# Performance work log

Measured on AMD Instinct MI355X. Metric: run time of the kernel, lower is better.

Reference implementation:

```python
import jax, jax.numpy as jnp
import numpy as np

N = 100000      # nodes
E = 1600000     # edges (avg degree 16)
IN = 128        # in_channels == nf
NF = 128        # hidden width
OUT = 3         # out_channels
NEG = 0.02      # LeakyReLU slope
EPS = 1e-5      # GraphNorm eps


def setup_inputs() -> dict:
    key = jax.random.key(0)
    ks = jax.random.split(key, 12)
    x = jax.random.normal(ks[0], (N, IN), dtype=jnp.float32)
    edge_index = jax.random.randint(ks[1], (2, E), 0, N, dtype=jnp.int32)
    s = 1.0 / np.sqrt(NF)
    # 6 hidden SAGEConv layers (NF->NF), stacked
    Wl = jax.random.normal(ks[2], (6, NF, NF), dtype=jnp.float32) * s
    bl = jnp.zeros((6, NF), dtype=jnp.float32)
    Wr = jax.random.normal(ks[3], (6, NF, NF), dtype=jnp.float32) * s
    # final SAGEConv NF -> OUT
    Wl_out = jax.random.normal(ks[4], (OUT, NF), dtype=jnp.float32) * s
    bl_out = jnp.zeros((OUT,), dtype=jnp.float32)
    Wr_out = jax.random.normal(ks[5], (OUT, NF), dtype=jnp.float32) * s
    # GraphNorm params for the 6 hidden layers
    gamma = jnp.ones((6, NF), dtype=jnp.float32)
    beta = jnp.zeros((6, NF), dtype=jnp.float32)
    alpha = jnp.ones((6, NF), dtype=jnp.float32)  # mean_scale
    return {"x": x, "edge_index": edge_index, "Wl": Wl, "bl": bl, "Wr": Wr,
            "Wl_out": Wl_out, "bl_out": bl_out, "Wr_out": Wr_out,
            "gamma": gamma, "beta": beta, "alpha": alpha}


def _sage_conv(h, src, dst, W_l, b_l, W_r):
    # max-aggregate messages x_j = h[src] onto dst, then two linears
    m = jax.ops.segment_max(h[src], dst, num_segments=h.shape[0])
    m = jnp.where(jnp.isfinite(m), m, 0.0)  # empty segments -> 0
    return m @ W_l.T + b_l + h @ W_r.T


def _graph_norm(h, g, b, a):
    mean = jnp.mean(h, axis=0, keepdims=True)          # [1, NF]
    sub = h - a * mean
    var = jnp.mean(sub * sub, axis=0, keepdims=True)   # [1, NF]
    return g * sub * jax.lax.rsqrt(var + EPS) + b


def reference(x, edge_index, Wl, bl, Wr, Wl_out, bl_out, Wr_out, gamma, beta, alpha):
    src, dst = edge_index[0], edge_index[1]
    h = x
    for i in range(6):
        h = _sage_conv(h, src, dst, Wl[i], bl[i], Wr[i])
        h = _graph_norm(h, gamma[i], beta[i], alpha[i])
        h = jnp.where(h > 0, h, NEG * h)  # LeakyReLU(0.02); dropout p=0
    h = _sage_conv(h, src, dst, Wl_out, bl_out, Wr_out)
    return jnp.tanh(h) * 0.5
```

## Files before the change

kernel.cpp:

```cpp
#include <hip/hip_runtime.h>
#include <math.h>

#define NN 100000
#define NE 1600000
#define NF 128
#define NOUT 3
#define NEGS 0.02f
#define GEPS 1e-5f

typedef __attribute__((ext_vector_type(8))) short bf16x8;
typedef __attribute__((ext_vector_type(4))) float f32x4;

__device__ __forceinline__ unsigned short bf16_rn(float f) {
    unsigned u = __float_as_uint(f);
    unsigned r = u + 0x7FFFu + ((u >> 16) & 1u);
    return (unsigned short)(r >> 16);
}
__device__ __forceinline__ float bf16_tf(unsigned short h) {
    return __uint_as_float((unsigned)h << 16);
}
__device__ __forceinline__ unsigned pk2(float v) {
    unsigned short hi = bf16_rn(v);
    unsigned short lo = bf16_rn(v - bf16_tf(hi));
    return ((unsigned)hi << 16) | lo;
}
__device__ __forceinline__ float unpk(unsigned u) {
    return __uint_as_float(u & 0xFFFF0000u) + __uint_as_float(u << 16);
}

__global__ void k_hist(const int* __restrict__ dst, int* __restrict__ counts,
                       int* __restrict__ rank) {
    int i = blockIdx.x * blockDim.x + threadIdx.x;
    if (i < NE) rank[i] = atomicAdd(&counts[dst[i]], 1);
}

__global__ void k_scan1(const int* __restrict__ counts, int* __restrict__ bsums) {
    __shared__ int s[256];
    int i = blockIdx.x * 256 + threadIdx.x;
    s[threadIdx.x] = (i < NN) ? counts[i] : 0;
    __syncthreads();
    for (int off = 128; off > 0; off >>= 1) {
        if (threadIdx.x < off) s[threadIdx.x] += s[threadIdx.x + off];
        __syncthreads();
    }
    if (threadIdx.x == 0) bsums[blockIdx.x] = s[0];
}

__global__ void k_scan2(int* __restrict__ bsums, int nb) {
    __shared__ int s[512];
    int t = threadIdx.x;
    int v = (t < nb) ? bsums[t] : 0;
    s[t] = v;
    __syncthreads();
    for (int off = 1; off < 512; off <<= 1) {
        int u = (t >= off) ? s[t - off] : 0;
        __syncthreads();
        s[t] += u;
        __syncthreads();
    }
    if (t < nb) bsums[t] = s[t] - v;
}

__global__ void k_scan3(const int* __restrict__ counts, const int* __restrict__ bsums,
                        int* __restrict__ offsets) {
    __shared__ int s[256];
    int i = blockIdx.x * 256 + threadIdx.x;
    int v = (i < NN) ? counts[i] : 0;
    s[threadIdx.x] = v;
    __syncthreads();
    for (int off = 1; off < 256; off <<= 1) {
        int u = (threadIdx.x >= off) ? s[threadIdx.x - off] : 0;
        __syncthreads();
        s[threadIdx.x] += u;
        __syncthreads();
    }
    int excl = s[threadIdx.x] - v + bsums[blockIdx.x];
    if (i <= NN) offsets[i] = excl;
}

__global__ void k_scatter(const int* __restrict__ src, const int* __restrict__ dst,
                          const int* __restrict__ offsets, const int* __restrict__ rank,
                          int* __restrict__ csr) {
    int i = blockIdx.x * blockDim.x + threadIdx.x;
    if (i < NE) csr[offsets[dst[i]] + rank[i]] = src[i];
}

__global__ void k_wsplit(const float* __restrict__ Wl, const float* __restrict__ Wr,
                         unsigned short* __restrict__ whi, unsigned short* __restrict__ wlo) {
    int i = blockIdx.x * 256 + threadIdx.x;
    if (i >= 6 * NF * 256) return;
    int L = i >> 15;
    int rem = i & 32767;
    int o = rem >> 8;
    int k = rem & 255;
    float v = (k < NF) ? Wl[L * NF * NF + o * NF + k] : Wr[L * NF * NF + o * NF + (k - NF)];
    unsigned short h = bf16_rn(v);
    whi[i] = h;
    wlo[i] = bf16_rn(v - bf16_tf(h));
}

__global__ void k_xpack(const float* __restrict__ x, unsigned* __restrict__ hpk) {
    int i = blockIdx.x * 256 + threadIdx.x;
    float4 v = ((const float4*)x)[i];
    uint4 p;
    p.x = pk2(v.x); p.y = pk2(v.y); p.z = pk2(v.z); p.w = pk2(v.w);
    ((uint4*)hpk)[i] = p;
}

__global__ __launch_bounds__(256) void k_aggmax(const unsigned* __restrict__ hpk,
                                                const int* __restrict__ offsets,
                                                const int* __restrict__ csr,
                                                unsigned* __restrict__ mpk) {
    int node = blockIdx.x * 4 + (threadIdx.x >> 6);
    int l = threadIdx.x & 63;
    int beg = offsets[node], end = offsets[node + 1];
    float aa = -INFINITY, ab = -INFINITY;
    int e = beg;
    for (; e + 8 <= end; e += 8) {
        int s0 = csr[e],     s1 = csr[e + 1], s2 = csr[e + 2], s3 = csr[e + 3];
        int s4 = csr[e + 4], s5 = csr[e + 5], s6 = csr[e + 6], s7 = csr[e + 7];
        uint2 g0 = *(const uint2*)&hpk[(size_t)s0 * NF + 2 * l];
        uint2 g1 = *(const uint2*)&hpk[(size_t)s1 * NF + 2 * l];
        uint2 g2 = *(const uint2*)&hpk[(size_t)s2 * NF + 2 * l];
        uint2 g3 = *(const uint2*)&hpk[(size_t)s3 * NF + 2 * l];
        uint2 g4 = *(const uint2*)&hpk[(size_t)s4 * NF + 2 * l];
        uint2 g5 = *(const uint2*)&hpk[(size_t)s5 * NF + 2 * l];
        uint2 g6 = *(const uint2*)&hpk[(size_t)s6 * NF + 2 * l];
        uint2 g7 = *(const uint2*)&hpk[(size_t)s7 * NF + 2 * l];
        float m0 = fmaxf(fmaxf(unpk(g0.x), unpk(g1.x)), fmaxf(unpk(g2.x), unpk(g3.x)));
        float m1 = fmaxf(fmaxf(unpk(g4.x), unpk(g5.x)), fmaxf(unpk(g6.x), unpk(g7.x)));
        float n0 = fmaxf(fmaxf(unpk(g0.y), unpk(g1.y)), fmaxf(unpk(g2.y), unpk(g3.y)));
        float n1 = fmaxf(fmaxf(unpk(g4.y), unpk(g5.y)), fmaxf(unpk(g6.y), unpk(g7.y)));
        aa = fmaxf(aa, fmaxf(m0, m1));
        ab = fmaxf(ab, fmaxf(n0, n1));
    }
    for (; e + 4 <= end; e += 4) {
        int s0 = csr[e], s1 = csr[e + 1], s2 = csr[e + 2], s3 = csr[e + 3];
        uint2 g0 = *(const uint2*)&hpk[(size_t)s0 * NF + 2 * l];
        uint2 g1 = *(const uint2*)&hpk[(size_t)s1 * NF + 2 * l];
        uint2 g2 = *(const uint2*)&hpk[(size_t)s2 * NF + 2 * l];
        uint2 g3 = *(const uint2*)&hpk[(size_t)s3 * NF + 2 * l];
        aa = fmaxf(aa, fmaxf(fmaxf(unpk(g0.x), unpk(g1.x)), fmaxf(unpk(g2.x), unpk(g3.x))));
        ab = fmaxf(ab, fmaxf(fmaxf(unpk(g0.y), unpk(g1.y)), fmaxf(unpk(g2.y), unpk(g3.y))));
    }
    for (; e < end; ++e) {
        uint2 g = *(const uint2*)&hpk[(size_t)csr[e] * NF + 2 * l];
        aa = fmaxf(aa, unpk(g.x));
        ab = fmaxf(ab, unpk(g.y));
    }
    uint2 r;
    r.x = (beg == end) ? 0u : pk2(aa);
    r.y = (beg == end) ? 0u : pk2(ab);
    *(uint2*)&mpk[(size_t)node * NF + 2 * l] = r;
}

__global__ __launch_bounds__(512) void k_gemm(const unsigned* __restrict__ mpk,
                                              const unsigned* __restrict__ hpk,
                                              const unsigned short* __restrict__ whi,
                                              const unsigned short* __restrict__ wlo,
                                              const float* __restrict__ bias,
                                              unsigned* __restrict__ zpk,
                                              float* __restrict__ stats) {
    __shared__ __align__(16) unsigned short wlds[32768];
    __shared__ float redS[64], redQ[64];
    const int tid = threadIdx.x;
    const int half = blockIdx.y;
    const int w = tid >> 6;
    const int l = tid & 63;
    const int arow = l & 15;
    const int kg = l >> 4;

    if (tid < 64) { redS[tid] = 0.f; redQ[tid] = 0.f; }

#pragma unroll
    for (int i = 0; i < 8; i++) {
        int gd = tid + i * 512;
        int arr = gd >> 11;
        int rem = gd & 2047;
        int nt = rem >> 9;
        int ks = (rem >> 6) & 7;
        int ls = rem & 63;
        int r = nt * 16 + (ls & 15);
        int g = ks * 4 + (ls >> 4);
        const unsigned short* srcw = arr ? wlo : whi;
        bf16x8 v = *(const bf16x8*)&srcw[(size_t)(half * 64 + r) * 256 + g * 8];
        *(bf16x8*)&wlds[arr * 16384 + rem * 8] = v;
    }
    __syncthreads();

    const int nbase = blockIdx.x * 256 + w * 32;
    int an0 = nbase + arow;      if (an0 > NN - 1) an0 = NN - 1;
    int an1 = nbase + 16 + arow; if (an1 > NN - 1) an1 = NN - 1;

    f32x4 acc0[4], acc1[4];
#pragma unroll
    for (int nt = 0; nt < 4; nt++) {
        acc0[nt] = (f32x4){0.f, 0.f, 0.f, 0.f};
        acc1[nt] = (f32x4){0.f, 0.f, 0.f, 0.f};
    }

    union U { uint4 u; bf16x8 v; };

#pragma unroll
    for (int ks = 0; ks < 8; ks++) {
        const unsigned* A = (ks < 4) ? mpk : hpk;
        const int ak = (ks & 3) * 32 + kg * 8;
        uint4 p0 = *(const uint4*)&A[(size_t)an0 * NF + ak];
        uint4 p1 = *(const uint4*)&A[(size_t)an0 * NF + ak + 4];
        uint4 q0 = *(const uint4*)&A[(size_t)an1 * NF + ak];
        uint4 q1 = *(const uint4*)&A[(size_t)an1 * NF + ak + 4];

        U ah0, al0, ah1, al1;
        ah0.u.x = (p0.x >> 16) | (p0.y & 0xFFFF0000u);
        ah0.u.y = (p0.z >> 16) | (p0.w & 0xFFFF0000u);
        ah0.u.z = (p1.x >> 16) | (p1.y & 0xFFFF0000u);
        ah0.u.w = (p1.z >> 16) | (p1.w & 0xFFFF0000u);
        al0.u.x = (p0.x & 0xFFFFu) | (p0.y << 16);
        al0.u.y = (p0.z & 0xFFFFu) | (p0.w << 16);
        al0.u.z = (p1.x & 0xFFFFu) | (p1.y << 16);
        al0.u.w = (p1.z & 0xFFFFu) | (p1.w << 16);
        ah1.u.x = (q0.x >> 16) | (q0.y & 0xFFFF0000u);
        ah1.u.y = (q0.z >> 16) | (q0.w & 0xFFFF0000u);
        ah1.u.z = (q1.x >> 16) | (q1.y & 0xFFFF0000u);
        ah1.u.w = (q1.z >> 16) | (q1.w & 0xFFFF0000u);
        al1.u.x = (q0.x & 0xFFFFu) | (q0.y << 16);
        al1.u.y = (q0.z & 0xFFFFu) | (q0.w << 16);
        al1.u.z = (q1.x & 0xFFFFu) | (q1.y << 16);
        al1.u.w = (q1.z & 0xFFFFu) | (q1.w << 16);

        bf16x8 bh[4], bl[4];
#pragma unroll
        for (int nt = 0; nt < 4; nt++) {
            int el = (nt * 512 + ks * 64 + l) * 8;
            bh[nt] = *(const bf16x8*)&wlds[el];
            bl[nt] = *(const bf16x8*)&wlds[16384 + el];
        }
#pragma unroll
        for (int nt = 0; nt < 4; nt++) {
            acc0[nt] = __builtin_amdgcn_mfma_f32_16x16x32_bf16(ah0.v, bh[nt], acc0[nt], 0, 0, 0);
            acc1[nt] = __builtin_amdgcn_mfma_f32_16x16x32_bf16(ah1.v, bh[nt], acc1[nt], 0, 0, 0);
        }
#pragma unroll
        for (int nt = 0; nt < 4; nt++) {
            acc0[nt] = __builtin_amdgcn_mfma_f32_16x16x32_bf16(ah0.v, bl[nt], acc0[nt], 0, 0, 0);
            acc1[nt] = __builtin_amdgcn_mfma_f32_16x16x32_bf16(ah1.v, bl[nt], acc1[nt], 0, 0, 0);
        }
#pragma unroll
        for (int nt = 0; nt < 4; nt++) {
            acc0[nt] = __builtin_amdgcn_mfma_f32_16x16x32_bf16(al0.v, bh[nt], acc0[nt], 0, 0, 0);
            acc1[nt] = __builtin_amdgcn_mfma_f32_16x16x32_bf16(al1.v, bh[nt], acc1[nt], 0, 0, 0);
        }
    }

#pragma unroll
    for (int nt = 0; nt < 4; nt++) {
        const int f = half * 64 + nt * 16 + arow;
        const float b = bias[f];
        float s = 0.f, q = 0.f;
#pragma unroll
        for (int r = 0; r < 4; r++) {
            int n0 = nbase + kg * 4 + r;
            float v0 = acc0[nt][r] + b;
            if (n0 < NN) { zpk[(size_t)n0 * NF + f] = pk2(v0); s += v0; q += v0 * v0; }
            int n1 = nbase + 16 + kg * 4 + r;
            float v1 = acc1[nt][r] + b;
            if (n1 < NN) { zpk[(size_t)n1 * NF + f] = pk2(v1); s += v1; q += v1 * v1; }
        }
        s += __shfl_xor(s, 16); s += __shfl_xor(s, 32);
        q += __shfl_xor(q, 16); q += __shfl_xor(q, 32);
        if (l < 16) {
            atomicAdd(&redS[nt * 16 + l], s);
            atomicAdd(&redQ[nt * 16 + l], q);
        }
    }
    __syncthreads();
    if (tid < 64) {
        atomicAdd(&stats[half * 64 + tid], redS[tid]);
        atomicAdd(&stats[NF + half * 64 + tid], redQ[tid]);
    }
}

__global__ __launch_bounds__(256) void k_norm(const float* __restrict__ stats,
                                              const float* __restrict__ gamma,
                                              const float* __restrict__ beta,
                                              const float* __restrict__ alpha,
                                              const unsigned* __restrict__ zpk,
                                              unsigned* __restrict__ hpk) {
    __shared__ float sc[NF], sh[NF];
    int tid = threadIdx.x;
    if (tid < NF) {
        float mean = stats[tid] * (1.0f / NN);
        float ex2 = stats[NF + tid] * (1.0f / NN);
        float a = alpha[tid];
        float am = a * mean;
        float var = ex2 - 2.f * am * mean + am * am;
        float inv = rsqrtf(var + GEPS);
        float g = gamma[tid] * inv;
        sc[tid] = g;
        sh[tid] = beta[tid] - g * am;
    }
    __syncthreads();
    int i = blockIdx.x * 256 + tid;
    uint4 z = ((const uint4*)zpk)[i];
    int f = (i & 31) * 4;
    float r0 = sc[f + 0] * unpk(z.x) + sh[f + 0]; r0 = r0 > 0.f ? r0 : NEGS * r0;
    float r1 = sc[f + 1] * unpk(z.y) + sh[f + 1]; r1 = r1 > 0.f ? r1 : NEGS * r1;
    float r2 = sc[f + 2] * unpk(z.z) + sh[f + 2]; r2 = r2 > 0.f ? r2 : NEGS * r2;
    float r3 = sc[f + 3] * unpk(z.w) + sh[f + 3]; r3 = r3 > 0.f ? r3 : NEGS * r3;
    uint4 p;
    p.x = pk2(r0); p.y = pk2(r1); p.z = pk2(r2); p.w = pk2(r3);
    ((uint4*)hpk)[i] = p;
}

__global__ __launch_bounds__(256) void k_final(const unsigned* __restrict__ mpk,
                                               const unsigned* __restrict__ hpk,
                                               const float* __restrict__ Wlo_,
                                               const float* __restrict__ blo_,
                                               const float* __restrict__ Wro_,
                                               float* __restrict__ out) {
    __shared__ __align__(16) float W[NOUT][256];
    __shared__ float bb[NOUT];
    int tid = threadIdx.x;
    for (int i = tid; i < NOUT * 256; i += 256) {
        int o = i >> 8, k = i & 255;
        W[o][k] = (k < NF) ? Wlo_[o * NF + k] : Wro_[o * NF + (k - NF)];
    }
    if (tid < NOUT) bb[tid] = blo_[tid];
    __syncthreads();

    int node = blockIdx.x * 64 + (tid >> 2);
    int j = tid & 3;
    if (node >= NN) return;
    const unsigned* sp = (j < 2) ? mpk : hpk;
    int kbase = (j & 1) * 64;
    const unsigned* rp = &sp[(size_t)node * NF + kbase];
    float a0 = 0.f, a1 = 0.f, a2 = 0.f;
#pragma unroll
    for (int q = 0; q < 16; q++) {
        uint4 u = *(const uint4*)&rp[q * 4];
        float v0 = unpk(u.x), v1 = unpk(u.y), v2 = unpk(u.z), v3 = unpk(u.w);
        int k = j * 64 + q * 4;
        float4 w0 = *(const float4*)&W[0][k];
        float4 w1 = *(const float4*)&W[1][k];
        float4 w2 = *(const float4*)&W[2][k];
        a0 += v0 * w0.x + v1 * w0.y + v2 * w0.z + v3 * w0.w;
        a1 += v0 * w1.x + v1 * w1.y + v2 * w1.z + v3 * w1.w;
        a2 += v0 * w2.x + v1 * w2.y + v2 * w2.z + v3 * w2.w;
    }
    a0 += __shfl_down(a0, 2, 4); a0 += __shfl_down(a0, 1, 4);
    a1 += __shfl_down(a1, 2, 4); a1 += __shfl_down(a1, 1, 4);
    a2 += __shfl_down(a2, 2, 4); a2 += __shfl_down(a2, 1, 4);
    if (j == 0) {
        out[node * 3 + 0] = tanhf(a0 + bb[0]) * 0.5f;
        out[node * 3 + 1] = tanhf(a1 + bb[1]) * 0.5f;
        out[node * 3 + 2] = tanhf(a2 + bb[2]) * 0.5f;
    }
}

extern "C" void kernel_launch(void* const* d_in, const int* in_sizes, int n_in,
                              void* d_out, int out_size, void* d_ws, size_t ws_size,
                              hipStream_t stream) {
    const float* x     = (const float*)d_in[0];
    const int*   ei    = (const int*)d_in[1];
    const float* Wl    = (const float*)d_in[2];
    const float* bl    = (const float*)d_in[3];
    const float* Wr    = (const float*)d_in[4];
    const float* Wlo   = (const float*)d_in[5];
    const float* blo   = (const float*)d_in[6];
    const float* Wro   = (const float*)d_in[7];
    const float* gamma = (const float*)d_in[8];
    const float* beta  = (const float*)d_in[9];
    const float* alpha = (const float*)d_in[10];
    float* out = (float*)d_out;

    const int* esrc = ei;
    const int* edst = ei + NE;

    char* ws = (char*)d_ws;
    size_t off = 0;
    auto alloc = [&](size_t bytes) -> void* {
        void* p = ws + off;
        off += (bytes + 255) & ~(size_t)255;
        return p;
    };

    const int NB = (NN + 255) / 256;
    int*      counts  = (int*)alloc(NN * sizeof(int));
    int*      offsets = (int*)alloc((NN + 1) * sizeof(int));
    int*      bsums   = (int*)alloc(NB * sizeof(int));
    int*      rank    = (int*)alloc(NE * sizeof(int));
    int*      csr     = (int*)alloc(NE * sizeof(int));
    unsigned* mpk     = (unsigned*)alloc((size_t)NN * NF * 4);
    unsigned* hpk     = (unsigned*)alloc((size_t)NN * NF * 4);
    unsigned* zpk     = (unsigned*)alloc((size_t)NN * NF * 4);
    unsigned short* whi6 = (unsigned short*)alloc((size_t)6 * NF * 256 * 2);
    unsigned short* wlo6 = (unsigned short*)alloc((size_t)6 * NF * 256 * 2);
    float*    stats   = (float*)alloc(6 * 2 * NF * sizeof(float));

    hipMemsetAsync(counts, 0, NN * sizeof(int), stream);
    hipMemsetAsync(stats, 0, 6 * 2 * NF * sizeof(float), stream);

    k_hist<<<(NE + 255) / 256, 256, 0, stream>>>(edst, counts, rank);
    k_scan1<<<NB, 256, 0, stream>>>(counts, bsums);
    k_scan2<<<1, 512, 0, stream>>>(bsums, NB);
    k_scan3<<<NB, 256, 0, stream>>>(counts, bsums, offsets);
    k_scatter<<<(NE + 255) / 256, 256, 0, stream>>>(esrc, edst, offsets, rank, csr);

    k_wsplit<<<(6 * NF * 256 + 255) / 256, 256, 0, stream>>>(Wl, Wr, whi6, wlo6);
    k_xpack<<<NN * NF / 4 / 256, 256, 0, stream>>>(x, hpk);

    const int aggGrid   = NN / 4;
    const int gemmGridX = (NN + 255) / 256;
    const int normGrid  = NN * NF / 4 / 256;
    const int finGrid   = (NN + 63) / 64;

    for (int L = 0; L < 6; ++L) {
        k_aggmax<<<aggGrid, 256, 0, stream>>>(hpk, offsets, csr, mpk);
        k_gemm<<<dim3(gemmGridX, 2), 512, 0, stream>>>(mpk, hpk,
                                                       whi6 + (size_t)L * NF * 256,
                                                       wlo6 + (size_t)L * NF * 256,
                                                       bl + (size_t)L * NF,
                                                       zpk, stats + (size_t)L * 2 * NF);
        k_norm<<<normGrid, 256, 0, stream>>>(stats + (size_t)L * 2 * NF,
                                             gamma + (size_t)L * NF,
                                             beta + (size_t)L * NF,
                                             alpha + (size_t)L * NF,
                                             zpk, hpk);
    }
    k_aggmax<<<aggGrid, 256, 0, stream>>>(hpk, offsets, csr, mpk);
    k_final<<<finGrid, 256, 0, stream>>>(mpk, hpk, Wlo, blo, Wro, out);
}
```

Baseline: 1.506 ms.

## Fuse GraphNorm+LeakyReLU into aggregation and GEMM, drop norm pass

Removes the standalone normalization kernel. The next layer's aggregation applies the per-feature scale/shift and LeakyReLU to the max-reduced values; this is valid because the affine map is monotone when gamma is positive. The GEMM applies the same transform when it loads the self features. The GEMM also now computes all 128 output columns per block instead of splitting into two halves, which doubles its LDS weight footprint and accumulator registers. A tiny kernel computes scale/shift from the stats, and ping-pong buffers replace the z/h pair. This saves a full read+write pass over the activations per layer, at the cost of more ALU work in the gather and lower GEMM occupancy.

```diff
diff --git a/kernel.cpp b/kernel.cpp
--- a/kernel.cpp
+++ b/kernel.cpp
@@ -99,17 +99,40 @@
     wlo[i] = bf16_rn(v - bf16_tf(h));
 }
 
-__global__ void k_xpack(const float* __restrict__ x, unsigned* __restrict__ hpk) {
+__global__ void k_xpack(const float* __restrict__ x, unsigned* __restrict__ zpk) {
     int i = blockIdx.x * 256 + threadIdx.x;
     float4 v = ((const float4*)x)[i];
     uint4 p;
     p.x = pk2(v.x); p.y = pk2(v.y); p.z = pk2(v.z); p.w = pk2(v.w);
-    ((uint4*)hpk)[i] = p;
-}
-
-__global__ __launch_bounds__(256) void k_aggmax(const unsigned* __restrict__ hpk,
+    ((uint4*)zpk)[i] = p;
+}
+
+__global__ void k_ident(float* __restrict__ scsh) {
+    int f = threadIdx.x;
+    scsh[f] = 1.0f;
+    scsh[NF + f] = 0.0f;
+}
+
+__global__ void k_scsh(const float* __restrict__ stats, const float* __restrict__ gamma,
+                       const float* __restrict__ beta, const float* __restrict__ alpha,
+                       float* __restrict__ scsh) {
+    int f = threadIdx.x;
+    float mean = stats[f] * (1.0f / NN);
+    float ex2 = stats[NF + f] * (1.0f / NN);
+    float a = alpha[f];
+    float am = a * mean;
+    float var = ex2 - 2.f * am * mean + am * am;
+    float inv = rsqrtf(var + GEPS);
+    float g = gamma[f] * inv;
+    scsh[f] = g;
+    scsh[NF + f] = beta[f] - g * am;
+}
+
+__global__ __launch_bounds__(256) void k_aggmax(const unsigned* __restrict__ zin,
                                                 const int* __restrict__ offsets,
                                                 const int* __restrict__ csr,
+                                                const float* __restrict__ scsh,
+                                                float neg,
                                                 unsigned* __restrict__ mpk) {
     int node = blockIdx.x * 4 + (threadIdx.x >> 6);
     int l = threadIdx.x & 63;
@@ -119,14 +142,14 @@
     for (; e + 8 <= end; e += 8) {
         int s0 = csr[e],     s1 = csr[e + 1], s2 = csr[e + 2], s3 = csr[e + 3];
         int s4 = csr[e + 4], s5 = csr[e + 5], s6 = csr[e + 6], s7 = csr[e + 7];
-        uint2 g0 = *(const uint2*)&hpk[(size_t)s0 * NF + 2 * l];
-        uint2 g1 = *(const uint2*)&hpk[(size_t)s1 * NF + 2 * l];
-        uint2 g2 = *(const uint2*)&hpk[(size_t)s2 * NF + 2 * l];
-        uint2 g3 = *(const uint2*)&hpk[(size_t)s3 * NF + 2 * l];
-        uint2 g4 = *(const uint2*)&hpk[(size_t)s4 * NF + 2 * l];
-        uint2 g5 = *(const uint2*)&hpk[(size_t)s5 * NF + 2 * l];
-        uint2 g6 = *(const uint2*)&hpk[(size_t)s6 * NF + 2 * l];
-        uint2 g7 = *(const uint2*)&hpk[(size_t)s7 * NF + 2 * l];
+        uint2 g0 = *(const uint2*)&zin[(size_t)s0 * NF + 2 * l];
+        uint2 g1 = *(const uint2*)&zin[(size_t)s1 * NF + 2 * l];
+        uint2 g2 = *(const uint2*)&zin[(size_t)s2 * NF + 2 * l];
+        uint2 g3 = *(const uint2*)&zin[(size_t)s3 * NF + 2 * l];
+        uint2 g4 = *(const uint2*)&zin[(size_t)s4 * NF + 2 * l];
+        uint2 g5 = *(const uint2*)&zin[(size_t)s5 * NF + 2 * l];
+        uint2 g6 = *(const uint2*)&zin[(size_t)s6 * NF + 2 * l];
+        uint2 g7 = *(const uint2*)&zin[(size_t)s7 * NF + 2 * l];
         float m0 = fmaxf(fmaxf(unpk(g0.x), unpk(g1.x)), fmaxf(unpk(g2.x), unpk(g3.x)));
         float m1 = fmaxf(fmaxf(unpk(g4.x), unpk(g5.x)), fmaxf(unpk(g6.x), unpk(g7.x)));
         float n0 = fmaxf(fmaxf(unpk(g0.y), unpk(g1.y)), fmaxf(unpk(g2.y), unpk(g3.y)));
@@ -134,57 +157,78 @@
         aa = fmaxf(aa, fmaxf(m0, m1));
         ab = fmaxf(ab, fmaxf(n0, n1));
     }
-    for (; e + 4 <= end; e += 4) {
-        int s0 = csr[e], s1 = csr[e + 1], s2 = csr[e + 2], s3 = csr[e + 3];
-        uint2 g0 = *(const uint2*)&hpk[(size_t)s0 * NF + 2 * l];
-        uint2 g1 = *(const uint2*)&hpk[(size_t)s1 * NF + 2 * l];
-        uint2 g2 = *(const uint2*)&hpk[(size_t)s2 * NF + 2 * l];
-        uint2 g3 = *(const uint2*)&hpk[(size_t)s3 * NF + 2 * l];
-        aa = fmaxf(aa, fmaxf(fmaxf(unpk(g0.x), unpk(g1.x)), fmaxf(unpk(g2.x), unpk(g3.x))));
-        ab = fmaxf(ab, fmaxf(fmaxf(unpk(g0.y), unpk(g1.y)), fmaxf(unpk(g2.y), unpk(g3.y))));
-    }
     for (; e < end; ++e) {
-        uint2 g = *(const uint2*)&hpk[(size_t)csr[e] * NF + 2 * l];
+        uint2 g = *(const uint2*)&zin[(size_t)csr[e] * NF + 2 * l];
         aa = fmaxf(aa, unpk(g.x));
         ab = fmaxf(ab, unpk(g.y));
     }
     uint2 r;
-    r.x = (beg == end) ? 0u : pk2(aa);
-    r.y = (beg == end) ? 0u : pk2(ab);
+    if (beg == end) {
+        r.x = 0u; r.y = 0u;
+    } else {
+        float sc0 = scsh[2 * l],      sc1 = scsh[2 * l + 1];
+        float sh0 = scsh[NF + 2 * l], sh1 = scsh[NF + 2 * l + 1];
+        float va = fmaf(sc0, aa, sh0); va = va > 0.f ? va : neg * va;
+        float vb = fmaf(sc1, ab, sh1); vb = vb > 0.f ? vb : neg * vb;
+        r.x = pk2(va); r.y = pk2(vb);
+    }
     *(uint2*)&mpk[(size_t)node * NF + 2 * l] = r;
 }
 
-__global__ __launch_bounds__(512) void k_gemm(const unsigned* __restrict__ mpk,
-                                              const unsigned* __restrict__ hpk,
+__device__ __forceinline__ void norm_unpack(uint4 a, uint4 b, const float* sc, const float* sh,
+                                            float neg, bf16x8* ah, bf16x8* al) {
+    unsigned uu[8] = {a.x, a.y, a.z, a.w, b.x, b.y, b.z, b.w};
+    unsigned hw[8], lw[8];
+#pragma unroll
+    for (int j = 0; j < 8; j++) {
+        float v = fmaf(sc[j], unpk(uu[j]), sh[j]);
+        v = v > 0.f ? v : neg * v;
+        unsigned short h = bf16_rn(v);
+        hw[j] = h;
+        lw[j] = bf16_rn(v - bf16_tf(h));
+    }
+    union U { uint4 u; bf16x8 v; } H, L;
+    H.u.x = hw[0] | (hw[1] << 16); H.u.y = hw[2] | (hw[3] << 16);
+    H.u.z = hw[4] | (hw[5] << 16); H.u.w = hw[6] | (hw[7] << 16);
+    L.u.x = lw[0] | (lw[1] << 16); L.u.y = lw[2] | (lw[3] << 16);
+    L.u.z = lw[4] | (lw[5] << 16); L.u.w = lw[6] | (lw[7] << 16);
+    *ah = H.v; *al = L.v;
+}
+
+__global__ __launch_bounds__(512) void k_gemm(const unsigned* __restrict__ zin,
+                                              const unsigned* __restrict__ mpk,
                                               const unsigned short* __restrict__ whi,
                                               const unsigned short* __restrict__ wlo,
                                               const float* __restrict__ bias,
-                                              unsigned* __restrict__ zpk,
+                                              const float* __restrict__ scsh,
+                                              float neg,
+                                              unsigned* __restrict__ zout,
                                               float* __restrict__ stats) {
-    __shared__ __align__(16) unsigned short wlds[32768];
-    __shared__ float redS[64], redQ[64];
+    __shared__ __align__(16) unsigned short wlds[65536];
+    __shared__ float slds[2 * NF];
+    __shared__ float redS[NF], redQ[NF];
     const int tid = threadIdx.x;
-    const int half = blockIdx.y;
     const int w = tid >> 6;
     const int l = tid & 63;
     const int arow = l & 15;
     const int kg = l >> 4;
 
-    if (tid < 64) { redS[tid] = 0.f; redQ[tid] = 0.f; }
-
-#pragma unroll
-    for (int i = 0; i < 8; i++) {
+    if (tid < NF) { redS[tid] = 0.f; redQ[tid] = 0.f; }
+    if (tid >= 256 && tid < 512) slds[tid - 256] = scsh[tid - 256];
+
+#pragma unroll
+    for (int i = 0; i < 16; i++) {
         int gd = tid + i * 512;
-        int arr = gd >> 11;
-        int rem = gd & 2047;
+        int arr = gd >> 12;
+        int rem = gd & 4095;
         int nt = rem >> 9;
         int ks = (rem >> 6) & 7;
         int ls = rem & 63;
         int r = nt * 16 + (ls & 15);
         int g = ks * 4 + (ls >> 4);
         const unsigned short* srcw = arr ? wlo : whi;
-        bf16x8 v = *(const bf16x8*)&srcw[(size_t)(half * 64 + r) * 256 + g * 8];
-        *(bf16x8*)&wlds[arr * 16384 + rem * 8] = v;
+        bf16x8 v = *(const bf16x8*)&srcw[(size_t)r * 256 + g * 8];
+        *(bf16x8*)&wlds[arr * 32768 + rem * 8] = v;
     }
     __syncthreads();
 
@@ -192,9 +236,9 @@
     int an0 = nbase + arow;      if (an0 > NN - 1) an0 = NN - 1;
     int an1 = nbase + 16 + arow; if (an1 > NN - 1) an1 = NN - 1;
 
-    f32x4 acc0[4], acc1[4];
-#pragma unroll
-    for (int nt = 0; nt < 4; nt++) {
+    f32x4 acc0[8], acc1[8];
+#pragma unroll
+    for (int nt = 0; nt < 8; nt++) {
         acc0[nt] = (f32x4){0.f, 0.f, 0.f, 0.f};
         acc1[nt] = (f32x4){0.f, 0.f, 0.f, 0.f};
     }
@@ -203,135 +247,108 @@
 
 #pragma unroll
     for (int ks = 0; ks < 8; ks++) {
-        const unsigned* A = (ks < 4) ? mpk : hpk;
         const int ak = (ks & 3) * 32 + kg * 8;
-        uint4 p0 = *(const uint4*)&A[(size_t)an0 * NF + ak];
-        uint4 p1 = *(const uint4*)&A[(size_t)an0 * NF + ak + 4];
-        uint4 q0 = *(const uint4*)&A[(size_t)an1 * NF + ak];
-        uint4 q1 = *(const uint4*)&A[(size_t)an1 * NF + ak + 4];
-
-        U ah0, al0, ah1, al1;
-        ah0.u.x = (p0.x >> 16) | (p0.y & 0xFFFF0000u);
-        ah0.u.y = (p0.z >> 16) | (p0.w & 0xFFFF0000u);
-        ah0.u.z = (p1.x >> 16) | (p1.y & 0xFFFF0000u);
-        ah0.u.w = (p1.z >> 16) | (p1.w & 0xFFFF0000u);
-        al0.u.x = (p0.x & 0xFFFFu) | (p0.y << 16);
-        al0.u.y = (p0.z & 0xFFFFu) | (p0.w << 16);
-        al0.u.z = (p1.x & 0xFFFFu) | (p1.y << 16);
-        al0.u.w = (p1.z & 0xFFFFu) | (p1.w << 16);
-        ah1.u.x = (q0.x >> 16) | (q0.y & 0xFFFF0000u);
-        ah1.u.y = (q0.z >> 16) | (q0.w & 0xFFFF0000u);
-        ah1.u.z = (q1.x >> 16) | (q1.y & 0xFFFF0000u);
-        ah1.u.w = (q1.z >> 16) | (q1.w & 0xFFFF0000u);
-        al1.u.x = (q0.x & 0xFFFFu) | (q0.y << 16);
-        al1.u.y = (q0.z & 0xFFFFu) | (q0.w << 16);
-        al1.u.z = (q1.x & 0xFFFFu) | (q1.y << 16);
-        al1.u.w = (q1.z & 0xFFFFu) | (q1.w << 16);
-
-        bf16x8 bh[4], bl[4];
-#pragma unroll
-        for (int nt = 0; nt < 4; nt++) {
+        bf16x8 ah0, al0, ah1, al1;
+        if (ks < 4) {
+            uint4 p0 = *(const uint4*)&mpk[(size_t)an0 * NF + ak];
+            uint4 p1 = *(const uint4*)&mpk[(size_t)an0 * NF + ak + 4];
+            uint4 q0 = *(const uint4*)&mpk[(size_t)an1 * NF + ak];
+            uint4 q1 = *(const uint4*)&mpk[(size_t)an1 * NF + ak + 4];
+            U H0, L0, H1, L1;
+            H0.u.x = (p0.x >> 16) | (p0.y & 0xFFFF0000u);
+            H0.u.y = (p0.z >> 16) | (p0.w & 0xFFFF0000u);
+            H0.u.z = (p1.x >> 16) | (p1.y & 0xFFFF0000u);
+            H0.u.w = (p1.z >> 16) | (p1.w & 0xFFFF0000u);
+            L0.u.x = (p0.x & 0xFFFFu) | (p0.y << 16);
+            L0.u.y = (p0.z & 0xFFFFu) | (p0.w << 16);
+            L0.u.z = (p1.x & 0xFFFFu) | (p1.y << 16);
+            L0.u.w = (p1.z & 0xFFFFu) | (p1.w << 16);
+            H1.u.x = (q0.x >> 16) | (q0.y & 0xFFFF0000u);
+            H1.u.y = (q0.z >> 16) | (q0.w & 0xFFFF0000u);
+            H1.u.z = (q1.x >> 16) | (q1.y & 0xFFFF0000u);
+            H1.u.w = (q1.z >> 16) | (q1.w & 0xFFFF0000u);
+            L1.u.x = (q0.x & 0xFFFFu) | (q0.y << 16);
+            L1.u.y = (q0.z & 0xFFFFu) | (q0.w << 16);
+            L1.u.z = (q1.x & 0xFFFFu) | (q1.y << 16);
+            L1.u.w = (q1.z & 0xFFFFu) | (q1.w << 16);
+            ah0 = H0.v; al0 = L0.v; ah1 = H1.v; al1 = L1.v;
+        } else {
+            uint4 p0 = *(const uint4*)&zin[(size_t)an0 * NF + ak];
+            uint4 p1 = *(const uint4*)&zin[(size_t)an0 * NF + ak + 4];
+            uint4 q0 = *(const uint4*)&zin[(size_t)an1 * NF + ak];
+            uint4 q1 = *(const uint4*)&zin[(size_t)an1 * NF + ak + 4];
+            float scv[8], shv[8];
+#pragma unroll
+            for (int j = 0; j < 8; j++) { scv[j] = slds[ak + j]; shv[j] = slds[NF + ak + j]; }
+            norm_unpack(p0, p1, scv, shv, neg, &ah0, &al0);
+            norm_unpack(q0, q1, scv, shv, neg, &ah1, &al1);
+        }
+
+#pragma unroll
+        for (int nt = 0; nt < 8; nt++) {
             int el = (nt * 512 + ks * 64 + l) * 8;
-            bh[nt] = *(const bf16x8*)&wlds[el];
-            bl[nt] = *(const bf16x8*)&wlds[16384 + el];
+            bf16x8 bh = *(const bf16x8*)&wlds[el];
+            bf16x8 bl = *(const bf16x8*)&wlds[32768 + el];
+            acc0[nt] = __builtin_amdgcn_mfma_f32_16x16x32_bf16(ah0, bh, acc0[nt], 0, 0, 0);
+            acc1[nt] = __builtin_amdgcn_mfma_f32_16x16x32_bf16(ah1, bh, acc1[nt], 0, 0, 0);
+            acc0[nt] = __builtin_amdgcn_mfma_f32_16x16x32_bf16(ah0, bl, acc0[nt], 0, 0, 0);
+            acc1[nt] = __builtin_amdgcn_mfma_f32_16x16x32_bf16(ah1, bl, acc1[nt], 0, 0, 0);
+            acc0[nt] = __builtin_amdgcn_mfma_f32_16x16x32_bf16(al0, bh, acc0[nt], 0, 0, 0);
+            acc1[nt] = __builtin_amdgcn_mfma_f32_16x16x32_bf16(al1, bh, acc1[nt], 0, 0, 0);
         }
-#pragma unroll
-        for (int nt = 0; nt < 4; nt++) {
-            acc0[nt] = __builtin_amdgcn_mfma_f32_16x16x32_bf16(ah0.v, bh[nt], acc0[nt], 0, 0, 0);
-            acc1[nt] = __builtin_amdgcn_mfma_f32_16x16x32_bf16(ah1.v, bh[nt], acc1[nt], 0, 0, 0);
-        }
-#pragma unroll
-        for (int nt = 0; nt < 4; nt++) {
-            acc0[nt] = __builtin_amdgcn_mfma_f32_16x16x32_bf16(ah0.v, bl[nt], acc0[nt], 0, 0, 0);
-            acc1[nt] = __builtin_amdgcn_mfma_f32_16x16x32_bf16(ah1.v, bl[nt], acc1[nt], 0, 0, 0);
-        }
-#pragma unroll
-        for (int nt = 0; nt < 4; nt++) {
-            acc0[nt] = __builtin_amdgcn_mfma_f32_16x16x32_bf16(al0.v, bh[nt], acc0[nt], 0, 0, 0);
-            acc1[nt] = __builtin_amdgcn_mfma_f32_16x16x32_bf16(al1.v, bh[nt], acc1[nt], 0, 0, 0);
-        }
-    }
-
-#pragma unroll
-    for (int nt = 0; nt < 4; nt++) {
-        const int f = half * 64 + nt * 16 + arow;
+    }
+
+#pragma unroll
+    for (int nt = 0; nt < 8; nt++) {
+        const int f = nt * 16 + arow;
         const float b = bias[f];
         float s = 0.f, q = 0.f;
 #pragma unroll
         for (int r = 0; r < 4; r++) {
             int n0 = nbase + kg * 4 + r;
             float v0 = acc0[nt][r] + b;
-            if (n0 < NN) { zpk[(size_t)n0 * NF + f] = pk2(v0); s += v0; q += v0 * v0; }
+            if (n0 < NN) { zout[(size_t)n0 * NF + f] = pk2(v0); s += v0; q += v0 * v0; }
             int n1 = nbase + 16 + kg * 4 + r;
             float v1 = acc1[nt][r] + b;
-            if (n1 < NN) { zpk[(size_t)n1 * NF + f] = pk2(v1); s += v1; q += v1 * v1; }
+            if (n1 < NN) { zout[(size_t)n1 * NF + f] = pk2(v1); s += v1; q += v1 * v1; }
         }
         s += __shfl_xor(s, 16); s += __shfl_xor(s, 32);
         q += __shfl_xor(q, 16); q += __shfl_xor(q, 32);
         if (l < 16) {
-            atomicAdd(&redS[nt * 16 + l], s);
-            atomicAdd(&redQ[nt * 16 + l], q);
+            atomicAdd(&redS[f], s);
+            atomicAdd(&redQ[f], q);
         }
     }
     __syncthreads();
-    if (tid < 64) {
-        atomicAdd(&stats[half * 64 + tid], redS[tid]);
-        atomicAdd(&stats[NF + half * 64 + tid], redQ[tid]);
-    }
-}
-
-__global__ __launch_bounds__(256) void k_norm(const float* __restrict__ stats,
-                                              const float* __restrict__ gamma,
-                                              const float* __restrict__ beta,
-                                              const float* __restrict__ alpha,
-                                              const unsigned* __restrict__ zpk,
-                                              unsigned* __restrict__ hpk) {
-    __shared__ float sc[NF], sh[NF];
-    int tid = threadIdx.x;
     if (tid < NF) {
-        float mean = stats[tid] * (1.0f / NN);
-        float ex2 = stats[NF + tid] * (1.0f / NN);
-        float a = alpha[tid];
-        float am = a * mean;
-        float var = ex2 - 2.f * am * mean + am * am;
-        float inv = rsqrtf(var + GEPS);
-        float g = gamma[tid] * inv;
-        sc[tid] = g;
-        sh[tid] = beta[tid] - g * am;
-    }
-    __syncthreads();
-    int i = blockIdx.x * 256 + tid;
-    uint4 z = ((const uint4*)zpk)[i];
-    int f = (i & 31) * 4;
-    float r0 = sc[f + 0] * unpk(z.x) + sh[f + 0]; r0 = r0 > 0.f ? r0 : NEGS * r0;
-    float r1 = sc[f + 1] * unpk(z.y) + sh[f + 1]; r1 = r1 > 0.f ? r1 : NEGS * r1;
-    float r2 = sc[f + 2] * unpk(z.z) + sh[f + 2]; r2 = r2 > 0.f ? r2 : NEGS * r2;
-    float r3 = sc[f + 3] * unpk(z.w) + sh[f + 3]; r3 = r3 > 0.f ? r3 : NEGS * r3;
-    uint4 p;
-    p.x = pk2(r0); p.y = pk2(r1); p.z = pk2(r2); p.w = pk2(r3);
-    ((uint4*)hpk)[i] = p;
+        atomicAdd(&stats[tid], redS[tid]);
+        atomicAdd(&stats[NF + tid], redQ[tid]);
+    }
 }
 
 __global__ __launch_bounds__(256) void k_final(const unsigned* __restrict__ mpk,
-                                               const unsigned* __restrict__ hpk,
+                                               const unsigned* __restrict__ zin,
+                                               const float* __restrict__ scsh,
                                                const float* __restrict__ Wlo_,
                                                const float* __restrict__ blo_,
                                                const float* __restrict__ Wro_,
                                                float* __restrict__ out) {
     __shared__ __align__(16) float W[NOUT][256];
     __shared__ float bb[NOUT];
+    __shared__ float sss[2 * NF];
     int tid = threadIdx.x;
     for (int i = tid; i < NOUT * 256; i += 256) {
         int o = i >> 8, k = i & 255;
         W[o][k] = (k < NF) ? Wlo_[o * NF + k] : Wro_[o * NF + (k - NF)];
     }
+    if (tid < 2 * NF) sss[tid] = scsh[tid];
     if (tid < NOUT) bb[tid] = blo_[tid];
     __syncthreads();
 
     int node = blockIdx.x * 64 + (tid >> 2);
     int j = tid & 3;
     if (node >= NN) return;
-    const unsigned* sp = (j < 2) ? mpk : hpk;
+    const unsigned* sp = (j < 2) ? mpk : zin;
     int kbase = (j & 1) * 64;
     const unsigned* rp = &sp[(size_t)node * NF + kbase];
     float a0 = 0.f, a1 = 0.f, a2 = 0.f;
@@ -340,6 +357,15 @@
         uint4 u = *(const uint4*)&rp[q * 4];
         float v0 = unpk(u.x), v1 = unpk(u.y), v2 = unpk(u.z), v3 = unpk(u.w);
         int k = j * 64 + q * 4;
+        if (j >= 2) {
+            int f = k - 128;
+            float4 scv = *(const float4*)&sss[f];
+            float4 shv = *(const float4*)&sss[NF + f];
+            v0 = fmaf(scv.x, v0, shv.x); v0 = v0 > 0.f ? v0 : NEGS * v0;
+            v1 = fmaf(scv.y, v1, shv.y); v1 = v1 > 0.f ? v1 : NEGS * v1;
+            v2 = fmaf(scv.z, v2, shv.z); v2 = v2 > 0.f ? v2 : NEGS * v2;
+            v3 = fmaf(scv.w, v3, shv.w); v3 = v3 > 0.f ? v3 : NEGS * v3;
+        }
         float4 w0 = *(const float4*)&W[0][k];
         float4 w1 = *(const float4*)&W[1][k];
         float4 w2 = *(const float4*)&W[2][k];
@@ -391,11 +417,12 @@
     int*      rank    = (int*)alloc(NE * sizeof(int));
     int*      csr     = (int*)alloc(NE * sizeof(int));
     unsigned* mpk     = (unsigned*)alloc((size_t)NN * NF * 4);
-    unsigned* hpk     = (unsigned*)alloc((size_t)NN * NF * 4);
-    unsigned* zpk     = (unsigned*)alloc((size_t)NN * NF * 4);
+    unsigned* zA      = (unsigned*)alloc((size_t)NN * NF * 4);
+    unsigned* zB      = (unsigned*)alloc((size_t)NN * NF * 4);
     unsigned short* whi6 = (unsigned short*)alloc((size_t)6 * NF * 256 * 2);
     unsigned short* wlo6 = (unsigned short*)alloc((size_t)6 * NF * 256 * 2);
     float*    stats   = (float*)alloc(6 * 2 * NF * sizeof(float));
+    float*    scsh    = (float*)alloc(7 * 2 * NF * sizeof(float));
 
     hipMemsetAsync(counts, 0, NN * sizeof(int), stream);
     hipMemsetAsync(stats, 0, 6 * 2 * NF * sizeof(float), stream);
@@ -407,26 +434,34 @@
     k_scatter<<<(NE + 255) / 256, 256, 0, stream>>>(esrc, edst, offsets, rank, csr);
 
     k_wsplit<<<(6 * NF * 256 + 255) / 256, 256, 0, stream>>>(Wl, Wr, whi6, wlo6);
-    k_xpack<<<NN * NF / 4 / 256, 256, 0, stream>>>(x, hpk);
+    k_xpack<<<NN * NF / 4 / 256, 256, 0, stream>>>(x, zA);
+    k_ident<<<1, 128, 0, stream>>>(scsh);
 
     const int aggGrid   = NN / 4;
     const int gemmGridX = (NN + 255) / 256;
-    const int normGrid  = NN * NF / 4 / 256;
     const int finGrid   = (NN + 63) / 64;
 
+    const unsigned* zin = zA;
+    unsigned* zot = zB;
     for (int L = 0; L < 6; ++L) {
-        k_aggmax<<<aggGrid, 256, 0, stream>>>(hpk, offsets, csr, mpk);
-        k_gemm<<<dim3(gemmGridX, 2), 512, 0, stream>>>(mpk, hpk,
-                                                       whi6 + (size_t)L * NF * 256,
-                                                       wlo6 + (size_t)L * NF * 256,
-                                                       bl + (size_t)L * NF,
-                                                       zpk, stats + (size_t)L * 2 * NF);
-        k_norm<<<normGrid, 256, 0, stream>>>(stats + (size_t)L * 2 * NF,
-                                             gamma + (size_t)L * NF,
-                                             beta + (size_t)L * NF,
-                                             alpha + (size_t)L * NF,
-                                             zpk, hpk);
-    }
-    k_aggmax<<<aggGrid, 256, 0, stream>>>(hpk, offsets, csr, mpk);
-    k_final<<<finGrid, 256, 0, stream>>>(mpk, hpk, Wlo, blo, Wro, out);
-}
+        float neg = (L == 0) ? 1.0f : NEGS;
+        k_aggmax<<<aggGrid, 256, 0, stream>>>(zin, offsets, csr,
+                                              scsh + (size_t)L * 2 * NF, neg, mpk);
+        k_gemm<<<gemmGridX, 512, 0, stream>>>(zin, mpk,
+                                              whi6 + (size_t)L * NF * 256,
+                                              wlo6 + (size_t)L * NF * 256,
+                                              bl + (size_t)L * NF,
+                                              scsh + (size_t)L * 2 * NF, neg,
+                                              zot, stats + (size_t)L * 2 * NF);
+        k_scsh<<<1, 128, 0, stream>>>(stats + (size_t)L * 2 * NF,
+                                      gamma + (size_t)L * NF,
+                                      beta + (size_t)L * NF,
+                                      alpha + (size_t)L * NF,
+                                      scsh + (size_t)(L + 1) * 2 * NF);
+        const unsigned* t = zin; zin = zot; zot = (unsigned*)t;
+    }
+    k_aggmax<<<aggGrid, 256, 0, stream>>>(zin, offsets, csr,
+                                          scsh + (size_t)6 * 2 * NF, NEGS, mpk);
+    k_final<<<finGrid, 256, 0, stream>>>(mpk, zin, scsh + (size_t)6 * 2 * NF,
+                                         Wlo, blo, Wro, out);
+}
```

Result: faster. 1.462 ms (-2.9%).
